# Optimization experiments

Hardware: AMD Instinct MI355X
Metric: run time of the kernel (lower is better)

## Reference

```python
import jax, jax.numpy as jnp
import numpy as np

NUM_GRAPHS = 512


def setup_inputs() -> dict:
    key = jax.random.key(0)
    ks = jax.random.split(key, 8)
    N, E, D, H = 50000, 800000, 128, 128
    x = jax.random.normal(ks[0], (N, D), dtype=jnp.float32)
    edge_attr = jax.random.normal(ks[1], (E, 8), dtype=jnp.float32)
    s = 1.0 / np.sqrt(D)
    W1 = jax.random.normal(ks[2], (D, H), dtype=jnp.float32) * s
    W2 = jax.random.normal(ks[3], (H, H), dtype=jnp.float32) * s
    W3 = jax.random.normal(ks[4], (H, H), dtype=jnp.float32) * s
    b1 = jnp.zeros((H,), jnp.float32)
    b2 = jnp.zeros((H,), jnp.float32)
    b3 = jnp.zeros((H,), jnp.float32)
    edge_index = jax.random.randint(ks[5], (2, E), 0, N, dtype=jnp.int64)
    batch = jnp.sort(jax.random.randint(ks[6], (N,), 0, NUM_GRAPHS, dtype=jnp.int64))
    return {"x": x, "edge_attr": edge_attr, "W1": W1, "b1": b1, "W2": W2,
            "b2": b2, "W3": W3, "b3": b3, "edge_index": edge_index, "batch": batch}


def reference(x, edge_attr, W1, b1, W2, b2, W3, b3, edge_index, batch):
    # edge_attr is accepted but unused (GCNConv ignores it), matching the source.
    N = x.shape[0]
    src, dst = edge_index[0], edge_index[1]
    loop = jnp.arange(N, dtype=src.dtype)
    src_f = jnp.concatenate([src, loop])  # self-loops appended (PyG GCNConv default)
    dst_f = jnp.concatenate([dst, loop])
    # symmetric degree normalization on A + I (deg >= 1 thanks to self-loops)
    deg = jax.ops.segment_sum(jnp.ones(src_f.shape[0], x.dtype), dst_f, num_segments=N)
    dinv = deg ** -0.5
    coef = (dinv[src_f] * dinv[dst_f])[:, None]  # [E+N, 1]

    def gcn_conv(h, W, b):
        h = h @ W                                   # linear first (PyG order)
        agg = jax.ops.segment_sum(h[src_f] * coef, dst_f, num_segments=N)
        return agg + b

    h = jax.nn.relu(gcn_conv(x, W1, b1))   # dropout is identity at inference
    h = jax.nn.relu(gcn_conv(h, W2, b2))
    h = jax.nn.relu(gcn_conv(h, W3, b3))

    # global_mean_pool over graph ids
    sums = jax.ops.segment_sum(h, batch, num_segments=NUM_GRAPHS)
    cnts = jax.ops.segment_sum(jnp.ones((N,), h.dtype), batch, num_segments=NUM_GRAPHS)
    return sums / jnp.maximum(cnts, 1.0)[:, None]
```

## Files before the change

kernel.cpp:

```cpp
#include <hip/hip_runtime.h>
#include <hip/hip_bf16.h>


#define TPB 256
#define CSTRIDE 16
#define RCAP 64
typedef unsigned short u16;
typedef unsigned int u32;
typedef __attribute__((ext_vector_type(8))) __bf16 bf16x8;
typedef __attribute__((ext_vector_type(8))) u16 u16x8;
typedef __attribute__((ext_vector_type(4))) float f32x4;

__device__ __forceinline__ u16 f2b(float f) {
    __bf16 b = (__bf16)f;
    return __builtin_bit_cast(u16, b);
}
__device__ __forceinline__ float b2f_lo(u32 w) { return __builtin_bit_cast(float, w << 16); }
__device__ __forceinline__ float b2f_hi(u32 w) { return __builtin_bit_cast(float, w & 0xffff0000u); }

__device__ __forceinline__ bf16x8 cvt8(float4 u0, float4 u1) {
    u16x8 r;
    r[0] = f2b(u0.x); r[1] = f2b(u0.y); r[2] = f2b(u0.z); r[3] = f2b(u0.w);
    r[4] = f2b(u1.x); r[5] = f2b(u1.y); r[6] = f2b(u1.z); r[7] = f2b(u1.w);
    return __builtin_bit_cast(bf16x8, r);
}

__device__ __forceinline__ void fillslot_body(int bid, const int* __restrict__ src,
                                              const int* __restrict__ dst,
                                              int* cursor, u16* __restrict__ colsF, int E) {
    int e = (bid * TPB + (int)threadIdx.x) * 4;
    if (e + 3 < E) {
        int4 s = *(const int4*)(src + e);
        int4 d = *(const int4*)(dst + e);
        int sl;
        sl = atomicAdd(&cursor[d.x * CSTRIDE], 1);
        if (sl < RCAP) colsF[(size_t)d.x * RCAP + sl] = (u16)s.x;
        sl = atomicAdd(&cursor[d.y * CSTRIDE], 1);
        if (sl < RCAP) colsF[(size_t)d.y * RCAP + sl] = (u16)s.y;
        sl = atomicAdd(&cursor[d.z * CSTRIDE], 1);
        if (sl < RCAP) colsF[(size_t)d.z * RCAP + sl] = (u16)s.z;
        sl = atomicAdd(&cursor[d.w * CSTRIDE], 1);
        if (sl < RCAP) colsF[(size_t)d.w * RCAP + sl] = (u16)s.w;
    } else {
        for (; e < E; ++e) {
            int sl = atomicAdd(&cursor[dst[e] * CSTRIDE], 1);
            if (sl < RCAP) colsF[(size_t)dst[e] * RCAP + sl] = (u16)src[e];
        }
    }
}

__device__ __forceinline__ void prepw_body(int bb, const float* __restrict__ Wa,
                                           const float* __restrict__ Wb,
                                           const float* __restrict__ Wc,
                                           u16* __restrict__ Wta, u16* __restrict__ Wtb,
                                           u16* __restrict__ Wtc) {
    int m = bb >> 3;
    const float* W = m == 0 ? Wa : (m == 1 ? Wb : Wc);
    u16* Wt = m == 0 ? Wta : (m == 1 ? Wtb : Wtc);
    int t = (bb & 7) * TPB + (int)threadIdx.x;
    int n = t >> 4, c = t & 15;
    u16x8 r;
#pragma unroll
    for (int j = 0; j < 8; ++j) r[j] = f2b(W[(8 * c + j) * 128 + n]);
    int cs = c ^ (n & 15);
    *(u16x8*)(Wt + n * 128 + cs * 8) = r;
}

__global__ __launch_bounds__(TPB) void k_zero_prep(int* cursor, int N, int nbZ4,
                                                   const float* __restrict__ Wa,
                                                   const float* __restrict__ Wb,
                                                   const float* __restrict__ Wc,
                                                   u16* __restrict__ Wta,
                                                   u16* __restrict__ Wtb,
                                                   u16* __restrict__ Wtc,
                                                   u16* __restrict__ bufA,
                                                   u16* __restrict__ bufB) {
    int b = blockIdx.x;
    if (b < nbZ4) {
        int i = b * TPB + (int)threadIdx.x;
        if (i < N * (CSTRIDE / 4)) ((int4*)cursor)[i] = (int4){0, 0, 0, 0};
    } else if (b < nbZ4 + 24) {
        prepw_body(b - nbZ4, Wa, Wb, Wc, Wta, Wtb, Wtc);
    } else {
        int t = threadIdx.x;
        uint4 z = (uint4){0, 0, 0, 0};
        if (t < 16) *(uint4*)(bufA + (size_t)N * 128 + t * 8) = z;
        else if (t < 32) *(uint4*)(bufB + (size_t)N * 128 + (t - 16) * 8) = z;
    }
}

template <bool F32IN, bool SCALE>
__device__ __forceinline__ void gemm_body(int bid, const void* __restrict__ Ain,
                                          const u16* __restrict__ Wt,
                                          u16* __restrict__ C, int N,
                                          const float* __restrict__ dinv) {
    __shared__ u16 Ws[128 * 128];
    int t = threadIdx.x;
    {
        const uint4* s = (const uint4*)Wt;
        uint4* d = (uint4*)Ws;
#pragma unroll
        for (int i = 0; i < 8; ++i) d[t + 256 * i] = s[t + 256 * i];
    }
    __syncthreads();
    int wave = t >> 6, lane = t & 63;
    int li = lane & 15, lq = lane >> 4;
    int r0 = bid * 128 + wave * 32;
    f32x4 acc[2][8];
#pragma unroll
    for (int i = 0; i < 2; ++i)
#pragma unroll
        for (int f = 0; f < 8; ++f) acc[i][f] = (f32x4){0.f, 0.f, 0.f, 0.f};

    int ra = r0 + li, rb = ra + 16;
    size_t ra_c = (size_t)(ra < N ? ra : N - 1);
    size_t rb_c = (size_t)(rb < N ? rb : N - 1);
#pragma unroll
    for (int kc = 0; kc < 4; ++kc) {
        int koff = 32 * kc + 8 * lq;
        bf16x8 a0, a1;
        if constexpr (F32IN) {
            const float* A = (const float*)Ain;
            const float4* p0 = (const float4*)(A + ra_c * 128 + koff);
            const float4* p1 = (const float4*)(A + rb_c * 128 + koff);
            a0 = cvt8(p0[0], p0[1]);
            a1 = cvt8(p1[0], p1[1]);
        } else {
            const u16* A = (const u16*)Ain;
            a0 = *(const bf16x8*)(A + ra_c * 128 + koff);
            a1 = *(const bf16x8*)(A + rb_c * 128 + koff);
        }
#pragma unroll
        for (int f = 0; f < 8; ++f) {
            int n = 16 * f + li;
            int chunk = (4 * kc + lq) ^ li;
            bf16x8 b = *(const bf16x8*)(Ws + n * 128 + chunk * 8);
            acc[0][f] = __builtin_amdgcn_mfma_f32_16x16x32_bf16(a0, b, acc[0][f], 0, 0, 0);
            acc[1][f] = __builtin_amdgcn_mfma_f32_16x16x32_bf16(a1, b, acc[1][f], 0, 0, 0);
        }
    }
#pragma unroll
    for (int ri = 0; ri < 2; ++ri)
#pragma unroll
        for (int r = 0; r < 4; ++r) {
            int row = r0 + 16 * ri + 4 * lq + r;
            if (row < N) {
                float dv = 1.0f;
                if constexpr (SCALE) dv = dinv[row];
#pragma unroll
                for (int f = 0; f < 8; ++f)
                    C[(size_t)row * 128 + 16 * f + li] = f2b(dv * acc[ri][f][r]);
            }
        }
}

template <bool F32IN, bool SCALE>
__global__ __launch_bounds__(TPB) void k_gemm(const void* __restrict__ Ain,
                                              const u16* __restrict__ Wt,
                                              u16* __restrict__ C, int N,
                                              const float* __restrict__ dinv) {
    gemm_body<F32IN, SCALE>(blockIdx.x, Ain, Wt, C, N, dinv);
}

__global__ __launch_bounds__(TPB) void k_gemm1_fill(const void* __restrict__ x,
                                                    const u16* __restrict__ Wt1,
                                                    u16* __restrict__ C, int N, int nbG,
                                                    const int* __restrict__ src,
                                                    const int* __restrict__ dst,
                                                    int* cursor, u16* __restrict__ colsF,
                                                    int E) {
    int b = blockIdx.x;
    if (b < nbG) {
        gemm_body<true, false>(b, x, Wt1, C, N, nullptr);
    } else {
        fillslot_body(b - nbG, src, dst, cursor, colsF, E);
    }
}

__global__ __launch_bounds__(TPB) void k_scale_dinv(const int* __restrict__ cursor,
                                                    float* __restrict__ dinv,
                                                    u16* __restrict__ g, int N) {
    int e8 = blockIdx.x * TPB + (int)threadIdx.x;
    if (e8 >= N * 16) return;
    int row = e8 >> 4;
    int off = (e8 & 15) * 8;
    float dv = 1.0f / sqrtf((float)(cursor[(size_t)row * CSTRIDE] + 1));
    if ((e8 & 15) == 0) dinv[row] = dv;
    u16* p = g + (size_t)row * 128 + off;
    uint4 v = *(uint4*)p;
    uint4 o;
    o.x = (u32)f2b(dv * b2f_lo(v.x)) | ((u32)f2b(dv * b2f_hi(v.x)) << 16);
    o.y = (u32)f2b(dv * b2f_lo(v.y)) | ((u32)f2b(dv * b2f_hi(v.y)) << 16);
    o.z = (u32)f2b(dv * b2f_lo(v.z)) | ((u32)f2b(dv * b2f_hi(v.z)) << 16);
    o.w = (u32)f2b(dv * b2f_lo(v.w)) | ((u32)f2b(dv * b2f_hi(v.w)) << 16);
    *(uint4*)p = o;
}

#define AGG_ISS(BUF, T)                                                    \
    {                                                                      \
        _Pragma("unroll") for (int u = 0; u < 8; ++u) {                    \
            int col = __shfl(cg[T], u, 8);                                 \
            const u16* p = g + (size_t)col * 128 + fo;                     \
            asm volatile("global_load_dwordx4 %0, %1, off sc0"             \
                         : "=v"(BUF[u]) : "v"(p));                         \
        }                                                                  \
    }
#define AGG_CONS(BUF)                                                      \
    {                                                                      \
        _Pragma("unroll") for (int u = 0; u < 8; ++u) {                    \
            a[0] += b2f_lo(BUF[u].x); a[1] += b2f_hi(BUF[u].x);            \
            a[2] += b2f_lo(BUF[u].y); a[3] += b2f_hi(BUF[u].y);            \
            a[4] += b2f_lo(BUF[u].z); a[5] += b2f_hi(BUF[u].z);            \
            a[6] += b2f_lo(BUF[u].w); a[7] += b2f_hi(BUF[u].w);            \
        }                                                                  \
    }
#define AGG_WAIT(n)                                                        \
    {                                                                      \
        asm volatile("s_waitcnt vmcnt(" #n ")" ::: "memory");              \
        __builtin_amdgcn_sched_barrier(0);                                 \
    }
#define AGG_STEP(T, CUR, NXT)                                              \
    if ((T) < nc) {                                                        \
        if ((T) + 1 < nc) { AGG_ISS(NXT, (T) + 1); AGG_WAIT(8); }          \
        else { AGG_WAIT(0); }                                              \
        AGG_CONS(CUR);                                                     \
    }

__global__ __launch_bounds__(TPB) void k_agg(const u16* __restrict__ g,
                                             const u16* __restrict__ colsF,
                                             const int* __restrict__ cursor,
                                             const float* __restrict__ dinv,
                                             const float* __restrict__ bias,
                                             u16* __restrict__ hout, int N, int hoff) {
    int node = blockIdx.x * 32 + ((int)threadIdx.x >> 3);
    int lane = threadIdx.x & 7;
    if (node >= N) return;
    int fo = hoff + lane * 8;
    int deg = cursor[(size_t)node * CSTRIDE];
    int end = deg < RCAP ? deg : RCAP;
    const u16* crow = colsF + (size_t)node * RCAP;
    float dn = dinv[node];
    float a[8];
    {
        uint4 vs = *(const uint4*)(g + (size_t)node * 128 + fo);
        a[0] = b2f_lo(vs.x); a[1] = b2f_hi(vs.x);
        a[2] = b2f_lo(vs.y); a[3] = b2f_hi(vs.y);
        a[4] = b2f_lo(vs.z); a[5] = b2f_hi(vs.z);
        a[6] = b2f_lo(vs.w); a[7] = b2f_hi(vs.w);
    }
    {
        int m = end;
        int cg[8];
#pragma unroll
        for (int q = 0; q < 8; ++q) {
            int off = 8 * q + lane;
            int c = (int)crow[off < m ? off : 0];
            cg[q] = (off < m) ? c : N;
        }
        int nc = (m + 7) >> 3;
        if (nc > 0) {
            uint4 vA[8], vB[8];
            AGG_ISS(vA, 0);
            AGG_STEP(0, vA, vB)
            AGG_STEP(1, vB, vA)
            AGG_STEP(2, vA, vB)
            AGG_STEP(3, vB, vA)
            AGG_STEP(4, vA, vB)
            AGG_STEP(5, vB, vA)
            AGG_STEP(6, vA, vB)
            AGG_STEP(7, vB, vA)
        }
    }
    const float4* bp = (const float4*)(bias + fo);
    float4 b0 = bp[0], b1 = bp[1];
    a[0] = fmaxf(fmaf(dn, a[0], b0.x), 0.f); a[1] = fmaxf(fmaf(dn, a[1], b0.y), 0.f);
    a[2] = fmaxf(fmaf(dn, a[2], b0.z), 0.f); a[3] = fmaxf(fmaf(dn, a[3], b0.w), 0.f);
    a[4] = fmaxf(fmaf(dn, a[4], b1.x), 0.f); a[5] = fmaxf(fmaf(dn, a[5], b1.y), 0.f);
    a[6] = fmaxf(fmaf(dn, a[6], b1.z), 0.f); a[7] = fmaxf(fmaf(dn, a[7], b1.w), 0.f);
    uint4 o;
    o.x = (u32)f2b(a[0]) | ((u32)f2b(a[1]) << 16);
    o.y = (u32)f2b(a[2]) | ((u32)f2b(a[3]) << 16);
    o.z = (u32)f2b(a[4]) | ((u32)f2b(a[5]) << 16);
    o.w = (u32)f2b(a[6]) | ((u32)f2b(a[7]) << 16);
    *(uint4*)(hout + (size_t)node * 128 + fo) = o;
}

__global__ __launch_bounds__(TPB) void k_pool(const u16* __restrict__ h,
                                              const int* __restrict__ batch,
                                              float* __restrict__ out, int N, int G) {
    int g = blockIdx.x;
    int w = threadIdx.x & 63;
    int rid = threadIdx.x >> 6;
    int beg, end;
    {
        int lo = 0, hi = N;
        while (lo < hi) { int m = (lo + hi) >> 1; if (batch[m] < g) lo = m + 1; else hi = m; }
        beg = lo;
        lo = 0; hi = N;
        int g1 = g + 1;
        while (lo < hi) { int m = (lo + hi) >> 1; if (batch[m] < g1) lo = m + 1; else hi = m; }
        end = lo;
    }
    const u32* h32 = (const u32*)h;
    float a0 = 0.f, a1 = 0.f;
#pragma unroll 2
    for (int n = beg + rid; n < end; n += 4) {
        u32 v = h32[(size_t)n * 64 + w];
        a0 += b2f_lo(v); a1 += b2f_hi(v);
    }
    __shared__ float red[4][64][2];
    red[rid][w][0] = a0;
    red[rid][w][1] = a1;
    __syncthreads();
    if (rid == 0) {
        a0 = red[0][w][0] + red[1][w][0] + red[2][w][0] + red[3][w][0];
        a1 = red[0][w][1] + red[1][w][1] + red[2][w][1] + red[3][w][1];
        int c = end - beg; if (c < 1) c = 1;
        float inv = 1.0f / (float)c;
        out[(size_t)g * 128 + 2 * w]     = a0 * inv;
        out[(size_t)g * 128 + 2 * w + 1] = a1 * inv;
    }
}

extern "C" void kernel_launch(void* const* d_in, const int* in_sizes, int n_in,
                              void* d_out, int out_size, void* d_ws, size_t ws_size,
                              hipStream_t stream) {
    const float* x  = (const float*)d_in[0];
    const float* W1 = (const float*)d_in[2];
    const float* b1 = (const float*)d_in[3];
    const float* W2 = (const float*)d_in[4];
    const float* b2 = (const float*)d_in[5];
    const float* W3 = (const float*)d_in[6];
    const float* b3 = (const float*)d_in[7];
    const int* ei    = (const int*)d_in[8];
    const int* batch = (const int*)d_in[9];

    int N = in_sizes[0] / 128;
    int E = in_sizes[8] / 2;
    int G = out_size / 128;
    const int* src = ei;
    const int* dst = ei + E;

    char* w = (char*)d_ws;
    auto alloc = [&](size_t bytes) -> void* {
        void* p = (void*)w;
        w += (bytes + 255) & ~(size_t)255;
        return p;
    };
    int*   cursor = (int*)alloc((size_t)N * CSTRIDE * 4);
    float* dinv   = (float*)alloc((size_t)N * 4);
    u16*   colsF  = (u16*)alloc((size_t)N * RCAP * 2);
    u16*   Wt1    = (u16*)alloc(128 * 128 * 2);
    u16*   Wt2    = (u16*)alloc(128 * 128 * 2);
    u16*   Wt3    = (u16*)alloc(128 * 128 * 2);
    u16*   bufA   = (u16*)alloc((size_t)(N + 1) * 128 * 2);
    u16*   bufB   = (u16*)alloc((size_t)(N + 1) * 128 * 2);

    int nbE4 = (E / 4 + TPB - 1) / TPB;
    int nbG = (N + 127) / 128;
    int nbZ4 = (N * (CSTRIDE / 4) + TPB - 1) / TPB;
    int nbS = (N * 16 + TPB - 1) / TPB;
    int nbA = (N + 31) / 32;

    k_zero_prep<<<nbZ4 + 24 + 1, TPB, 0, stream>>>(cursor, N, nbZ4, W1, W2, W3,
                                                   Wt1, Wt2, Wt3, bufA, bufB);
    k_gemm1_fill<<<nbG + nbE4, TPB, 0, stream>>>(x, Wt1, bufA, N, nbG,
                                                 src, dst, cursor, colsF, E);
    k_scale_dinv<<<nbS, TPB, 0, stream>>>(cursor, dinv, bufA, N);

    k_agg<<<nbA, TPB, 0, stream>>>(bufA, colsF, cursor, dinv, b1, bufB, N, 0);
    k_agg<<<nbA, TPB, 0, stream>>>(bufA, colsF, cursor, dinv, b1, bufB, N, 64);
    k_gemm<false, true><<<nbG, TPB, 0, stream>>>(bufB, Wt2, bufA, N, dinv);
    k_agg<<<nbA, TPB, 0, stream>>>(bufA, colsF, cursor, dinv, b2, bufB, N, 0);
    k_agg<<<nbA, TPB, 0, stream>>>(bufA, colsF, cursor, dinv, b2, bufB, N, 64);
    k_gemm<false, true><<<nbG, TPB, 0, stream>>>(bufB, Wt3, bufA, N, dinv);
    k_agg<<<nbA, TPB, 0, stream>>>(bufA, colsF, cursor, dinv, b3, bufB, N, 0);
    k_agg<<<nbA, TPB, 0, stream>>>(bufA, colsF, cursor, dinv, b3, bufB, N, 64);

    k_pool<<<G, TPB, 0, stream>>>(bufB, batch, (float*)d_out, N, G);
}
```

Baseline: 187.3 us.

## Merge feature-half aggregation launches and vectorize neighbor index loads

Each layer's aggregation used to be two separate launches, one per 64-column half of the features. These become one launch whose block index interleaves groups of four 32-node chunks with the two halves, so blocks covering the same nodes for both halves run close together and can share neighbor rows in cache. This also removes three launches and their tail gaps. Per-thread neighbor indices are now read with one 16-byte vector load and broadcast by shuffle, replacing eight scalar 2-byte loads, and the bound check moves into the issue loop. The trade-off is that the index load always reads all 64 slots, even for low-degree nodes.

```diff
diff --git a/kernel.cpp b/kernel.cpp
--- a/kernel.cpp
+++ b/kernel.cpp
@@ -199,7 +199,8 @@
 #define AGG_ISS(BUF, T)                                                    \
     {                                                                      \
         _Pragma("unroll") for (int u = 0; u < 8; ++u) {                    \
-            int col = __shfl(cg[T], u, 8);                                 \
+            int cc = __shfl(cv[u], T, 8);                                  \
+            int col = (8 * (T) + u < m) ? cc : N;                          \
             const u16* p = g + (size_t)col * 128 + fo;                     \
             asm volatile("global_load_dwordx4 %0, %1, off sc0"             \
                          : "=v"(BUF[u]) : "v"(p));                         \
@@ -231,14 +232,17 @@
                                              const int* __restrict__ cursor,
                                              const float* __restrict__ dinv,
                                              const float* __restrict__ bias,
-                                             u16* __restrict__ hout, int N, int hoff) {
-    int node = blockIdx.x * 32 + ((int)threadIdx.x >> 3);
+                                             u16* __restrict__ hout, int N) {
+    int b = blockIdx.x;
+    int x8 = b & 7;
+    int chunk = (b >> 3) * 4 + (x8 & 3);
+    int hoff = (x8 >> 2) * 64;
+    int node = chunk * 32 + ((int)threadIdx.x >> 3);
     int lane = threadIdx.x & 7;
     if (node >= N) return;
     int fo = hoff + lane * 8;
     int deg = cursor[(size_t)node * CSTRIDE];
-    int end = deg < RCAP ? deg : RCAP;
-    const u16* crow = colsF + (size_t)node * RCAP;
+    int m = deg < RCAP ? deg : RCAP;
     float dn = dinv[node];
     float a[8];
     {
@@ -249,14 +253,12 @@
         a[6] = b2f_lo(vs.w); a[7] = b2f_hi(vs.w);
     }
     {
-        int m = end;
-        int cg[8];
-#pragma unroll
-        for (int q = 0; q < 8; ++q) {
-            int off = 8 * q + lane;
-            int c = (int)crow[off < m ? off : 0];
-            cg[q] = (off < m) ? c : N;
-        }
+        uint4 cvec = *(const uint4*)(colsF + (size_t)node * RCAP + lane * 8);
+        int cv[8];
+        cv[0] = (int)(cvec.x & 0xffff); cv[1] = (int)(cvec.x >> 16);
+        cv[2] = (int)(cvec.y & 0xffff); cv[3] = (int)(cvec.y >> 16);
+        cv[4] = (int)(cvec.z & 0xffff); cv[5] = (int)(cvec.z >> 16);
+        cv[6] = (int)(cvec.w & 0xffff); cv[7] = (int)(cvec.w >> 16);
         int nc = (m + 7) >> 3;
         if (nc > 0) {
             uint4 vA[8], vB[8];
@@ -360,7 +362,8 @@
     int nbG = (N + 127) / 128;
     int nbZ4 = (N * (CSTRIDE / 4) + TPB - 1) / TPB;
     int nbS = (N * 16 + TPB - 1) / TPB;
-    int nbA = (N + 31) / 32;
+    int C32 = (N + 31) / 32;
+    int nbAgg = 2 * (((C32 + 3) / 4) * 4);
 
     k_zero_prep<<<nbZ4 + 24 + 1, TPB, 0, stream>>>(cursor, N, nbZ4, W1, W2, W3,
                                                    Wt1, Wt2, Wt3, bufA, bufB);
@@ -368,14 +371,11 @@
                                                  src, dst, cursor, colsF, E);
     k_scale_dinv<<<nbS, TPB, 0, stream>>>(cursor, dinv, bufA, N);
 
-    k_agg<<<nbA, TPB, 0, stream>>>(bufA, colsF, cursor, dinv, b1, bufB, N, 0);
-    k_agg<<<nbA, TPB, 0, stream>>>(bufA, colsF, cursor, dinv, b1, bufB, N, 64);
+    k_agg<<<nbAgg, TPB, 0, stream>>>(bufA, colsF, cursor, dinv, b1, bufB, N);
     k_gemm<false, true><<<nbG, TPB, 0, stream>>>(bufB, Wt2, bufA, N, dinv);
-    k_agg<<<nbA, TPB, 0, stream>>>(bufA, colsF, cursor, dinv, b2, bufB, N, 0);
-    k_agg<<<nbA, TPB, 0, stream>>>(bufA, colsF, cursor, dinv, b2, bufB, N, 64);
+    k_agg<<<nbAgg, TPB, 0, stream>>>(bufA, colsF, cursor, dinv, b2, bufB, N);
     k_gemm<false, true><<<nbG, TPB, 0, stream>>>(bufB, Wt3, bufA, N, dinv);
-    k_agg<<<nbA, TPB, 0, stream>>>(bufA, colsF, cursor, dinv, b3, bufB, N, 0);
-    k_agg<<<nbA, TPB, 0, stream>>>(bufA, colsF, cursor, dinv, b3, bufB, N, 64);
+    k_agg<<<nbAgg, TPB, 0, stream>>>(bufA, colsF, cursor, dinv, b3, bufB, N);
 
     k_pool<<<G, TPB, 0, stream>>>(bufB, batch, (float*)d_out, N, G);
 }
```

Result: faster. 167.0 us (-10.8%).
